# Optimization experiments

Measured on AMD Instinct MI355X. Metric: run time of the kernel, lower is better.

Reference implementation:

```python
import jax, jax.numpy as jnp
import numpy as np

B, NF, E, T, M = 4096, 50, 64, 2, 3
LN_EPS = 1e-5
NEG_INF = -1e9


def _xavier_uniform(k, shape, fan_in, fan_out):
    a = float(np.sqrt(6.0 / (fan_in + fan_out)))
    return jax.random.uniform(k, shape, jnp.float32, -a, a)


def setup_inputs() -> dict:
    key = jax.random.key(0)
    ks = jax.random.split(key, 6)
    feat = jax.random.normal(ks[0], (B, NF, E), jnp.float32)
    masker = _xavier_uniform(ks[1], (T, M, NF, NF), NF, NF)
    transform_w = _xavier_uniform(ks[2], (1, T, 1, 2 * E, E), 2 * E, E)
    transform_b = _xavier_uniform(ks[3], (T, 1, NF, E), NF, E)
    ln_w = jnp.ones((NF,), jnp.float32)
    ln_b = jnp.zeros((NF,), jnp.float32)
    gating_w = jax.random.normal(ks[4], (NF * E, 1), jnp.float32) / np.sqrt(NF * E)
    gating_b = jnp.zeros((1,), jnp.float32)
    return {
        "feat": feat,
        "masker": masker,
        "transform_w": transform_w,
        "transform_b": transform_b,
        "ln_w": ln_w,
        "ln_b": ln_b,
        "gating_w": gating_w,
        "gating_b": gating_b,
    }


def reference(feat, masker, transform_w, transform_b, ln_w, ln_b, gating_w, gating_b):
    b, nf, e = feat.shape
    t = masker.shape[0]
    # hop adjacency: product of masks, relu'd  (T, F, F)
    adj = jax.nn.relu(jnp.prod(masker, axis=1))
    mask = (adj != 0).astype(feat.dtype)
    # LayerNorm(num_fields) applied on transposed adj == normalize over axis -2,
    # with gamma/beta broadcasting along the normalized (row) axis.
    mean = adj.mean(axis=-2, keepdims=True)
    var = adj.var(axis=-2, keepdims=True)
    adj_ln = (adj - mean) / jnp.sqrt(var + LN_EPS) * ln_w[:, None] + ln_b[:, None]
    logits = adj_ln + (1.0 - mask) * NEG_INF + jnp.eye(nf, dtype=feat.dtype)
    # softmax over dim=1 of (T, F, F) == axis -2 (rows), then re-mask
    attn = jax.nn.softmax(logits, axis=-2) * mask
    # nei[b,t,g,e] = sum_f feat[b,f,e] * attn[t,f,g]
    nei = jnp.einsum('bfe,tfg->btge', feat, attn)  # (B, T, F, E)
    x = jnp.broadcast_to(feat[:, None], (b, t, nf, e))
    cat = jnp.concatenate([x, nei], axis=-1)  # (B, T, F, 2E)
    w0 = transform_w[0, :, 0]                 # (T, 2E, E)  (idx=0 slice)
    h = jnp.einsum('btfk,tke->btfe', cat, w0) + transform_b[:, 0]  # (B,T,F,E)
    flat = h.reshape(b, t, nf * e)
    gate = jax.nn.softmax(flat @ gating_w + gating_b, axis=1)  # (B, T, 1)
    out = jnp.sum(flat * gate, axis=1).reshape(b, nf, e)
    return out
```

## Files before the change

### kernel.cpp

```cpp
#include <hip/hip_runtime.h>
#include <hip/hip_bf16.h>

#define NFEAT 50
#define EDIM 64
#define LN_EPS 1e-5f
#define NEG_INF_C (-1000000000.0f)
#define NB 4

typedef __bf16 bf16_t;
typedef __bf16 bf16x8 __attribute__((ext_vector_type(8)));
typedef __bf16 bf16x4 __attribute__((ext_vector_type(4)));
typedef float f32x4 __attribute__((ext_vector_type(4)));


__global__ __launch_bounds__(256) void prep_kernel(
    const float* __restrict__ masker, const float* __restrict__ ln_w,
    const float* __restrict__ ln_b, const float* __restrict__ tw,
    const float* __restrict__ tb, const float* __restrict__ gw,
    bf16_t* __restrict__ ws_attnT, bf16_t* __restrict__ ws_WT,
    float* __restrict__ ws_tbT, float* __restrict__ ws_gwT,
    float* __restrict__ ws_cst)
{
  __shared__ float red[2][4];
  const int tid = threadIdx.x;
  const int lane = tid & 63;
  const int gidx = blockIdx.x * 256 + tid;

#pragma unroll
  for (int j = 0; j < 4; ++j) {
    int o = gidx * 4 + j;
    int kl = o & 63;
    int e = (o >> 6) & 63;
    int ti = o >> 12;
    int k = ((kl >> 3) ^ (e & 7)) * 8 + (kl & 7);
    ws_WT[o] = (bf16_t)tw[(ti * 64 + k) * 64 + e];
  }

#pragma unroll
  for (int j = 0; j < 2; ++j) {
    int o = gidx * 2 + j;
    int f = o & 63;
    int e = (o >> 6) & 63;
    int t = o >> 12;
    ws_tbT[o] = (f < NFEAT) ? tb[(t * NFEAT + f) * EDIM + e] : 0.f;
  }

  {
    int o = gidx;
    int f = o & 63;
    int e = o >> 6;
    ws_gwT[o] = (f < NFEAT) ? gw[f * EDIM + e] : 0.f;
  }

  if (blockIdx.x == 0) {
    float s0 = 0.f, s1 = 0.f;
    for (int i = tid; i < NFEAT * EDIM; i += 256) {
      float g = gw[i];
      s0 += tb[i] * g;
      s1 += tb[NFEAT * EDIM + i] * g;
    }
    for (int off = 32; off > 0; off >>= 1) {
      s0 += __shfl_xor(s0, off);
      s1 += __shfl_xor(s1, off);
    }
    if (lane == 0) { red[0][tid >> 6] = s0; red[1][tid >> 6] = s1; }
    __syncthreads();
    if (tid == 0) {
      ws_cst[0] = red[0][0] + red[0][1] + red[0][2] + red[0][3];
      ws_cst[1] = red[1][0] + red[1][1] + red[1][2] + red[1][3];
    }
  }

  const int wg = blockIdx.x * 4 + (tid >> 6);
  const int f = lane;
  const bool fv = (f < NFEAT);
  for (int i = 0; i < 2; ++i) {
    int col = wg * 2 + i;
    int t = col >> 6, g = col & 63;
    float val = 0.f;
    if (fv && g < NFEAT) {
      float a0 = masker[((t * 3 + 0) * NFEAT + f) * NFEAT + g];
      float a1 = masker[((t * 3 + 1) * NFEAT + f) * NFEAT + g];
      float a2 = masker[((t * 3 + 2) * NFEAT + f) * NFEAT + g];
      float prod = a0 * a1 * a2;
      val = prod > 0.f ? prod : 0.f;
    }
    float s = val;
    for (int off = 32; off > 0; off >>= 1) s += __shfl_xor(s, off);
    float mean = s / (float)NFEAT;
    float d = fv ? (val - mean) : 0.f;
    float v2 = d * d;
    for (int off = 32; off > 0; off >>= 1) v2 += __shfl_xor(v2, off);
    float var = v2 / (float)NFEAT;
    float lw = fv ? ln_w[f] : 0.f;
    float lb = fv ? ln_b[f] : 0.f;
    float aln = d * rsqrtf(var + LN_EPS) * lw + lb;
    float logit = aln + ((val != 0.f) ? 0.f : NEG_INF_C) + ((f == g) ? 1.f : 0.f);
    if (!fv) logit = -3.0e38f;
    float mx = logit;
    for (int off = 32; off > 0; off >>= 1) mx = fmaxf(mx, __shfl_xor(mx, off));
    float ex = fv ? expf(logit - mx) : 0.f;
    float se = ex;
    for (int off = 32; off > 0; off >>= 1) se += __shfl_xor(se, off);
    float attn = (fv && g < NFEAT && val != 0.f) ? (ex / se) : 0.f;
    ws_attnT[(t * 64 + g) * 64 + f] = (bf16_t)attn;
  }
}

__global__ __launch_bounds__(256) void main_kernel(
    const float* __restrict__ feat, const float* __restrict__ gb,
    const bf16_t* __restrict__ ws_attnT, const bf16_t* __restrict__ ws_WT,
    const float* __restrict__ ws_tbT, const float* __restrict__ ws_gwT,
    const float* __restrict__ ws_cst,
    float* __restrict__ out)
{
  __shared__ bf16_t sWT[4 * 64 * 64];
  __shared__ bf16_t sPT[2][64 * 72];
  __shared__ float sLog[2][4];

  const int tid = threadIdx.x;
  const int w = tid >> 6;
  const int lane = tid & 63;
  const int l16 = lane & 15;
  const int lquad = lane >> 4;
  const int m0 = w * 16;

#pragma unroll
  for (int it = 0; it < 8; ++it) {
    const int idx = it * 256 + tid;
    *(bf16x8*)&sWT[idx * 8] = *(const bf16x8*)(ws_WT + idx * 8);
  }

  bf16x8 aat[2][2];
#pragma unroll
  for (int t = 0; t < 2; ++t)
#pragma unroll
    for (int kc = 0; kc < 2; ++kc)
      aat[t][kc] = *(const bf16x8*)(ws_attnT + (t * 64 + m0 + l16) * 64 + kc * 32 + lquad * 8);

  const float cst0 = ws_cst[0], cst1 = ws_cst[1], gbv = gb[0];
  const int fA = m0 + l16;
  const bool fAv = (fA < NFEAT);
  const int b0 = blockIdx.x * NB;
  const int foff = fA * 64 + lquad * 8;
  const int exl = l16 & 7;

  f32x4 raw[4];
  if (fAv) {
    const float* fb = feat + b0 * (NFEAT * EDIM) + foff;
    raw[0] = *(const f32x4*)(fb);
    raw[1] = *(const f32x4*)(fb + 4);
    raw[2] = *(const f32x4*)(fb + 32);
    raw[3] = *(const f32x4*)(fb + 36);
  }

  __syncthreads();

#pragma unroll 1
  for (int ib = 0; ib < NB; ++ib) {
    const int b = b0 + ib;

    bf16x8 a[2];
#pragma unroll
    for (int kc = 0; kc < 2; ++kc)
#pragma unroll
      for (int j = 0; j < 8; ++j) a[kc][j] = (bf16_t)0.f;
    if (fAv) {
#pragma unroll
      for (int j = 0; j < 4; ++j) {
        a[0][j] = (bf16_t)raw[0][j]; a[0][j + 4] = (bf16_t)raw[1][j];
        a[1][j] = (bf16_t)raw[2][j]; a[1][j + 4] = (bf16_t)raw[3][j];
      }
    }

    if (ib + 1 < NB && fAv) {
      const float* fb = feat + (b + 1) * (NFEAT * EDIM) + foff;
      raw[0] = *(const f32x4*)(fb);
      raw[1] = *(const f32x4*)(fb + 4);
      raw[2] = *(const f32x4*)(fb + 32);
      raw[3] = *(const f32x4*)(fb + 36);
    }

    f32x4 accH[2][4], accP[2][4];
#pragma unroll
    for (int t = 0; t < 2; ++t)
#pragma unroll
      for (int n = 0; n < 4; ++n) {
        accH[t][n] = (f32x4){0.f, 0.f, 0.f, 0.f};
        accP[t][n] = (f32x4){0.f, 0.f, 0.f, 0.f};
      }

#pragma unroll
    for (int kc = 0; kc < 2; ++kc) {
      const int chunk = ((kc * 4 + lquad) ^ exl) * 8;
#pragma unroll
      for (int n = 0; n < 4; ++n) {
        const int ro = (n * 16 + l16) * 64 + chunk;
        const bf16x8 b10 = *(const bf16x8*)(&sWT[0 * 4096 + ro]);
        const bf16x8 b20 = *(const bf16x8*)(&sWT[1 * 4096 + ro]);
        const bf16x8 b11 = *(const bf16x8*)(&sWT[2 * 4096 + ro]);
        const bf16x8 b21 = *(const bf16x8*)(&sWT[3 * 4096 + ro]);
        accH[0][n] = __builtin_amdgcn_mfma_f32_16x16x32_bf16(a[kc], b10, accH[0][n], 0, 0, 0);
        accP[0][n] = __builtin_amdgcn_mfma_f32_16x16x32_bf16(a[kc], b20, accP[0][n], 0, 0, 0);
        accH[1][n] = __builtin_amdgcn_mfma_f32_16x16x32_bf16(a[kc], b11, accH[1][n], 0, 0, 0);
        accP[1][n] = __builtin_amdgcn_mfma_f32_16x16x32_bf16(a[kc], b21, accP[1][n], 0, 0, 0);
      }
    }

#pragma unroll
    for (int t = 0; t < 2; ++t)
#pragma unroll
      for (int n = 0; n < 4; ++n) {
        bf16x4 pv;
        pv[0] = (bf16_t)accP[t][n][0]; pv[1] = (bf16_t)accP[t][n][1];
        pv[2] = (bf16_t)accP[t][n][2]; pv[3] = (bf16_t)accP[t][n][3];
        *(bf16x4*)&sPT[t][(n * 16 + l16) * 72 + m0 + lquad * 4] = pv;
      }
    __syncthreads();

#pragma unroll
    for (int kc = 0; kc < 2; ++kc) {
#pragma unroll
      for (int n = 0; n < 4; ++n) {
        const int so = (n * 16 + l16) * 72 + kc * 32 + lquad * 8;
        const bf16x8 bp0 = *(const bf16x8*)(&sPT[0][so]);
        const bf16x8 bp1 = *(const bf16x8*)(&sPT[1][so]);
        accH[0][n] = __builtin_amdgcn_mfma_f32_16x16x32_bf16(aat[0][kc], bp0, accH[0][n], 0, 0, 0);
        accH[1][n] = __builtin_amdgcn_mfma_f32_16x16x32_bf16(aat[1][kc], bp1, accH[1][n], 0, 0, 0);
      }
    }

    float p0 = 0.f, p1 = 0.f;
#pragma unroll
    for (int n = 0; n < 4; ++n) {
      const f32x4 gwv = *(const f32x4*)(ws_gwT + (n * 16 + l16) * 64 + m0 + lquad * 4);
#pragma unroll
      for (int r = 0; r < 4; ++r) {
        p0 += accH[0][n][r] * gwv[r];
        p1 += accH[1][n][r] * gwv[r];
      }
    }
#pragma unroll
    for (int off = 32; off > 0; off >>= 1) {
      p0 += __shfl_xor(p0, off);
      p1 += __shfl_xor(p1, off);
    }
    if (lane == 0) { sLog[0][w] = p0; sLog[1][w] = p1; }
    __syncthreads();

    const float g0 = sLog[0][0] + sLog[0][1] + sLog[0][2] + sLog[0][3] + cst0 + gbv;
    const float g1 = sLog[1][0] + sLog[1][1] + sLog[1][2] + sLog[1][3] + cst1 + gbv;
    const float mx = fmaxf(g0, g1);
    const float e0 = expf(g0 - mx), e1 = expf(g1 - mx);
    const float inv = 1.f / (e0 + e1);
    const float ga0 = e0 * inv, ga1 = e1 * inv;

    float* outb = out + b * (NFEAT * EDIM);
#pragma unroll
    for (int n = 0; n < 4; ++n) {
      const int ro = (n * 16 + l16) * 64 + m0 + lquad * 4;
      const f32x4 tbv0 = *(const f32x4*)(ws_tbT + ro);
      const f32x4 tbv1 = *(const f32x4*)(ws_tbT + 64 * 64 + ro);
      const int e = n * 16 + l16;
#pragma unroll
      for (int r = 0; r < 4; ++r) {
        const int f = m0 + lquad * 4 + r;
        if (f < NFEAT)
          outb[f * 64 + e] = ga0 * (accH[0][n][r] + tbv0[r])
                           + ga1 * (accH[1][n][r] + tbv1[r]);
      }
    }
  }
}

extern "C" void kernel_launch(void* const* d_in, const int* in_sizes, int n_in,
                              void* d_out, int out_size, void* d_ws, size_t ws_size,
                              hipStream_t stream) {
  const float* feat   = (const float*)d_in[0];
  const float* masker = (const float*)d_in[1];
  const float* tw     = (const float*)d_in[2];
  const float* tb     = (const float*)d_in[3];
  const float* lnw    = (const float*)d_in[4];
  const float* lnb    = (const float*)d_in[5];
  const float* gw     = (const float*)d_in[6];
  const float* gb     = (const float*)d_in[7];
  float* out = (float*)d_out;

  bf16_t* ws_attnT = (bf16_t*)d_ws;
  bf16_t* ws_WT    = ws_attnT + 2 * 64 * 64;
  float*  ws_tbT   = (float*)(ws_WT + 4 * 64 * 64);
  float*  ws_gwT   = ws_tbT + 2 * 64 * 64;
  float*  ws_cst   = ws_gwT + 64 * 64;

  prep_kernel<<<16, 256, 0, stream>>>(masker, lnw, lnb, tw, tb, gw,
                                      ws_attnT, ws_WT, ws_tbT, ws_gwT, ws_cst);
  main_kernel<<<4096 / NB, 256, 0, stream>>>(feat, gb, ws_attnT, ws_WT,
                                             ws_tbT, ws_gwT, ws_cst, out);
}
```

Baseline: 138.1 us.

## Precompute gating projection matrix and split waves between H and P work

```diff
diff --git a/kernel.cpp b/kernel.cpp
--- a/kernel.cpp
+++ b/kernel.cpp
@@ -12,13 +12,15 @@
 typedef __bf16 bf16x4 __attribute__((ext_vector_type(4)));
 typedef float f32x4 __attribute__((ext_vector_type(4)));
 
+#define MFMA __builtin_amdgcn_mfma_f32_16x16x32_bf16
+
 
 __global__ __launch_bounds__(256) void prep_kernel(
     const float* __restrict__ masker, const float* __restrict__ ln_w,
     const float* __restrict__ ln_b, const float* __restrict__ tw,
     const float* __restrict__ tb, const float* __restrict__ gw,
     bf16_t* __restrict__ ws_attnT, bf16_t* __restrict__ ws_WT,
-    float* __restrict__ ws_tbT, float* __restrict__ ws_gwT,
+    float* __restrict__ ws_tbT, float* __restrict__ ws_attnF,
     float* __restrict__ ws_cst)
 {
   __shared__ float red[2][4];
@@ -43,13 +45,6 @@
     int e = (o >> 6) & 63;
     int t = o >> 12;
     ws_tbT[o] = (f < NFEAT) ? tb[(t * NFEAT + f) * EDIM + e] : 0.f;
-  }
-
-  {
-    int o = gidx;
-    int f = o & 63;
-    int e = o >> 6;
-    ws_gwT[o] = (f < NFEAT) ? gw[f * EDIM + e] : 0.f;
   }
 
   if (blockIdx.x == 0) {
@@ -104,26 +99,122 @@
     for (int off = 32; off > 0; off >>= 1) se += __shfl_xor(se, off);
     float attn = (fv && g < NFEAT && val != 0.f) ? (ex / se) : 0.f;
     ws_attnT[(t * 64 + g) * 64 + f] = (bf16_t)attn;
-  }
+    ws_attnF[(t * 64 + f) * 64 + g] = attn;
+  }
+}
+
+__global__ __launch_bounds__(256) void prep2_kernel(
+    const float* __restrict__ tw, const float* __restrict__ gw,
+    const float* __restrict__ ws_attnF, float* __restrict__ ws_G)
+{
+  __shared__ bf16_t sRT[64 * 72];
+  const int t = blockIdx.x;
+  const int tid = threadIdx.x;
+  const int w = tid >> 6;
+  const int lane = tid & 63;
+  const int l16 = lane & 15;
+  const int lquad = lane >> 4;
+  const int fr = w * 16 + l16;
+  const bool frv = (fr < NFEAT);
+
+  bf16x8 ag[2];
+#pragma unroll
+  for (int kc = 0; kc < 2; ++kc) {
+#pragma unroll
+    for (int j = 0; j < 8; ++j) ag[kc][j] = (bf16_t)0.f;
+    if (frv) {
+      const float* p = gw + fr * 64 + kc * 32 + lquad * 8;
+      const f32x4 r0 = *(const f32x4*)(p);
+      const f32x4 r1 = *(const f32x4*)(p + 4);
+#pragma unroll
+      for (int j = 0; j < 4; ++j) { ag[kc][j] = (bf16_t)r0[j]; ag[kc][j+4] = (bf16_t)r1[j]; }
+    }
+  }
+
+  f32x4 accR[4];
+#pragma unroll
+  for (int n = 0; n < 4; ++n) accR[n] = (f32x4){0.f,0.f,0.f,0.f};
+#pragma unroll
+  for (int kc = 0; kc < 2; ++kc)
+#pragma unroll
+    for (int n = 0; n < 4; ++n) {
+      const float* p = tw + ((2*t+1)*64 + n*16 + l16) * 64 + kc*32 + lquad*8;
+      const f32x4 r0 = *(const f32x4*)(p);
+      const f32x4 r1 = *(const f32x4*)(p + 4);
+      bf16x8 bw;
+#pragma unroll
+      for (int j = 0; j < 4; ++j) { bw[j] = (bf16_t)r0[j]; bw[j+4] = (bf16_t)r1[j]; }
+      accR[n] = MFMA(ag[kc], bw, accR[n], 0, 0, 0);
+    }
+#pragma unroll
+  for (int n = 0; n < 4; ++n) {
+    bf16x4 pv;
+    pv[0]=(bf16_t)accR[n][0]; pv[1]=(bf16_t)accR[n][1];
+    pv[2]=(bf16_t)accR[n][2]; pv[3]=(bf16_t)accR[n][3];
+    *(bf16x4*)&sRT[(n*16 + l16) * 72 + w*16 + lquad*4] = pv;
+  }
+
+  f32x4 acc[4];
+#pragma unroll
+  for (int n = 0; n < 4; ++n) acc[n] = (f32x4){0.f,0.f,0.f,0.f};
+#pragma unroll
+  for (int kc = 0; kc < 2; ++kc)
+#pragma unroll
+    for (int n = 0; n < 4; ++n) {
+      const float* p = tw + ((2*t)*64 + n*16 + l16) * 64 + kc*32 + lquad*8;
+      const f32x4 r0 = *(const f32x4*)(p);
+      const f32x4 r1 = *(const f32x4*)(p + 4);
+      bf16x8 bw;
+#pragma unroll
+      for (int j = 0; j < 4; ++j) { bw[j] = (bf16_t)r0[j]; bw[j+4] = (bf16_t)r1[j]; }
+      acc[n] = MFMA(ag[kc], bw, acc[n], 0, 0, 0);
+    }
+
+  __syncthreads();
+
+  bf16x8 aa[2];
+#pragma unroll
+  for (int kc = 0; kc < 2; ++kc) {
+    const float* p = ws_attnF + (t*64 + fr) * 64 + kc*32 + lquad*8;
+    const f32x4 r0 = *(const f32x4*)(p);
+    const f32x4 r1 = *(const f32x4*)(p + 4);
+#pragma unroll
+    for (int j = 0; j < 4; ++j) { aa[kc][j] = (bf16_t)r0[j]; aa[kc][j+4] = (bf16_t)r1[j]; }
+  }
+#pragma unroll
+  for (int kc = 0; kc < 2; ++kc)
+#pragma unroll
+    for (int n = 0; n < 4; ++n) {
+      const bf16x8 bp = *(const bf16x8*)(&sRT[(n*16 + l16) * 72 + kc*32 + lquad*8]);
+      acc[n] = MFMA(aa[kc], bp, acc[n], 0, 0, 0);
+    }
+
+#pragma unroll
+  for (int n = 0; n < 4; ++n)
+#pragma unroll
+    for (int r = 0; r < 4; ++r)
+      ws_G[t*4096 + (w*16 + lquad*4 + r) * 64 + n*16 + l16] = acc[n][r];
 }
 
 __global__ __launch_bounds__(256) void main_kernel(
     const float* __restrict__ feat, const float* __restrict__ gb,
     const bf16_t* __restrict__ ws_attnT, const bf16_t* __restrict__ ws_WT,
-    const float* __restrict__ ws_tbT, const float* __restrict__ ws_gwT,
+    const float* __restrict__ ws_tbT, const float* __restrict__ ws_G,
     const float* __restrict__ ws_cst,
     float* __restrict__ out)
 {
   __shared__ bf16_t sWT[4 * 64 * 64];
   __shared__ bf16_t sPT[2][64 * 72];
-  __shared__ float sLog[2][4];
+  __shared__ float sLog[2];
 
   const int tid = threadIdx.x;
   const int w = tid >> 6;
   const int lane = tid & 63;
   const int l16 = lane & 15;
   const int lquad = lane >> 4;
-  const int m0 = w * 16;
+  const bool isH = (w < 2);
+  const int pt = w - 2;
+  const int exl = l16 & 7;
 
 #pragma unroll
   for (int it = 0; it < 8; ++it) {
@@ -131,27 +222,40 @@
     *(bf16x8*)&sWT[idx * 8] = *(const bf16x8*)(ws_WT + idx * 8);
   }
 
-  bf16x8 aat[2][2];
-#pragma unroll
-  for (int t = 0; t < 2; ++t)
-#pragma unroll
-    for (int kc = 0; kc < 2; ++kc)
-      aat[t][kc] = *(const bf16x8*)(ws_attnT + (t * 64 + m0 + l16) * 64 + kc * 32 + lquad * 8);
+  bf16x8 aat[2][2][2];
+  if (isH) {
+#pragma unroll
+    for (int t = 0; t < 2; ++t)
+#pragma unroll
+      for (int kc = 0; kc < 2; ++kc)
+#pragma unroll
+        for (int ml = 0; ml < 2; ++ml)
+          aat[t][kc][ml] = *(const bf16x8*)(ws_attnT +
+              (t*64 + w*32 + ml*16 + l16) * 64 + kc*32 + lquad*8);
+  }
 
   const float cst0 = ws_cst[0], cst1 = ws_cst[1], gbv = gb[0];
-  const int fA = m0 + l16;
-  const bool fAv = (fA < NFEAT);
   const int b0 = blockIdx.x * NB;
-  const int foff = fA * 64 + lquad * 8;
-  const int exl = l16 & 7;
-
-  f32x4 raw[4];
-  if (fAv) {
-    const float* fb = feat + b0 * (NFEAT * EDIM) + foff;
-    raw[0] = *(const f32x4*)(fb);
-    raw[1] = *(const f32x4*)(fb + 4);
-    raw[2] = *(const f32x4*)(fb + 32);
-    raw[3] = *(const f32x4*)(fb + 36);
+  const int nm = isH ? 2 : 4;
+  const int fbase = isH ? w * 32 : 0;
+
+  f32x4 raw[16];
+#pragma unroll
+  for (int i = 0; i < 16; ++i) raw[i] = (f32x4){0.f,0.f,0.f,0.f};
+  {
+    const float* fb = feat + (long)b0 * (NFEAT * EDIM);
+#pragma unroll
+    for (int m = 0; m < 4; ++m)
+      if (m < nm) {
+        const int frow = fbase + m * 16 + l16;
+        if (frow < NFEAT) {
+          const float* p = fb + frow * 64 + lquad * 8;
+          raw[m*4+0] = *(const f32x4*)(p);
+          raw[m*4+1] = *(const f32x4*)(p + 4);
+          raw[m*4+2] = *(const f32x4*)(p + 32);
+          raw[m*4+3] = *(const f32x4*)(p + 36);
+        }
+      }
   }
 
   __syncthreads();
@@ -160,116 +264,141 @@
   for (int ib = 0; ib < NB; ++ib) {
     const int b = b0 + ib;
 
-    bf16x8 a[2];
+    bf16x8 a[2][4];
 #pragma unroll
     for (int kc = 0; kc < 2; ++kc)
 #pragma unroll
-      for (int j = 0; j < 8; ++j) a[kc][j] = (bf16_t)0.f;
-    if (fAv) {
-#pragma unroll
-      for (int j = 0; j < 4; ++j) {
-        a[0][j] = (bf16_t)raw[0][j]; a[0][j + 4] = (bf16_t)raw[1][j];
-        a[1][j] = (bf16_t)raw[2][j]; a[1][j + 4] = (bf16_t)raw[3][j];
+      for (int m = 0; m < 4; ++m)
+#pragma unroll
+        for (int j = 0; j < 4; ++j) {
+          a[kc][m][j]     = (bf16_t)raw[m*4 + kc*2][j];
+          a[kc][m][j + 4] = (bf16_t)raw[m*4 + kc*2 + 1][j];
+        }
+
+    if (!isH) {
+      const float* gt = ws_G + pt * 4096;
+      float p = 0.f;
+#pragma unroll
+      for (int m = 0; m < 4; ++m) {
+        const float* gp = gt + (m*16 + l16) * 64 + lquad * 8;
+        const f32x4 g0 = *(const f32x4*)(gp);
+        const f32x4 g1 = *(const f32x4*)(gp + 4);
+        const f32x4 g2 = *(const f32x4*)(gp + 32);
+        const f32x4 g3 = *(const f32x4*)(gp + 36);
+#pragma unroll
+        for (int j = 0; j < 4; ++j)
+          p += raw[m*4+0][j]*g0[j] + raw[m*4+1][j]*g1[j]
+             + raw[m*4+2][j]*g2[j] + raw[m*4+3][j]*g3[j];
       }
-    }
-
-    if (ib + 1 < NB && fAv) {
-      const float* fb = feat + (b + 1) * (NFEAT * EDIM) + foff;
-      raw[0] = *(const f32x4*)(fb);
-      raw[1] = *(const f32x4*)(fb + 4);
-      raw[2] = *(const f32x4*)(fb + 32);
-      raw[3] = *(const f32x4*)(fb + 36);
-    }
-
-    f32x4 accH[2][4], accP[2][4];
-#pragma unroll
-    for (int t = 0; t < 2; ++t)
-#pragma unroll
-      for (int n = 0; n < 4; ++n) {
-        accH[t][n] = (f32x4){0.f, 0.f, 0.f, 0.f};
-        accP[t][n] = (f32x4){0.f, 0.f, 0.f, 0.f};
+#pragma unroll
+      for (int off = 32; off > 0; off >>= 1) p += __shfl_xor(p, off);
+      if (lane == 0) sLog[pt] = p;
+    }
+
+    f32x4 acc[16];
+#pragma unroll
+    for (int i = 0; i < 16; ++i) acc[i] = (f32x4){0.f,0.f,0.f,0.f};
+
+    if (isH) {
+#pragma unroll
+      for (int kc = 0; kc < 2; ++kc) {
+        const int co = ((kc*4 + lquad) ^ exl) * 8;
+#pragma unroll
+        for (int n = 0; n < 4; ++n) {
+          const int ro = (n*16 + l16) * 64 + co;
+          const bf16x8 bw0 = *(const bf16x8*)(&sWT[0*4096 + ro]);
+          const bf16x8 bw1 = *(const bf16x8*)(&sWT[2*4096 + ro]);
+#pragma unroll
+          for (int ml = 0; ml < 2; ++ml) {
+            acc[ml*4 + n]     = MFMA(a[kc][ml], bw0, acc[ml*4 + n], 0, 0, 0);
+            acc[(2+ml)*4 + n] = MFMA(a[kc][ml], bw1, acc[(2+ml)*4 + n], 0, 0, 0);
+          }
+        }
       }
-
-#pragma unroll
-    for (int kc = 0; kc < 2; ++kc) {
-      const int chunk = ((kc * 4 + lquad) ^ exl) * 8;
-#pragma unroll
-      for (int n = 0; n < 4; ++n) {
-        const int ro = (n * 16 + l16) * 64 + chunk;
-        const bf16x8 b10 = *(const bf16x8*)(&sWT[0 * 4096 + ro]);
-        const bf16x8 b20 = *(const bf16x8*)(&sWT[1 * 4096 + ro]);
-        const bf16x8 b11 = *(const bf16x8*)(&sWT[2 * 4096 + ro]);
-        const bf16x8 b21 = *(const bf16x8*)(&sWT[3 * 4096 + ro]);
-        accH[0][n] = __builtin_amdgcn_mfma_f32_16x16x32_bf16(a[kc], b10, accH[0][n], 0, 0, 0);
-        accP[0][n] = __builtin_amdgcn_mfma_f32_16x16x32_bf16(a[kc], b20, accP[0][n], 0, 0, 0);
-        accH[1][n] = __builtin_amdgcn_mfma_f32_16x16x32_bf16(a[kc], b11, accH[1][n], 0, 0, 0);
-        accP[1][n] = __builtin_amdgcn_mfma_f32_16x16x32_bf16(a[kc], b21, accP[1][n], 0, 0, 0);
+    } else {
+      const int ti = 2*pt + 1;
+#pragma unroll
+      for (int kc = 0; kc < 2; ++kc) {
+        const int co = ((kc*4 + lquad) ^ exl) * 8;
+#pragma unroll
+        for (int n = 0; n < 4; ++n) {
+          const bf16x8 bw = *(const bf16x8*)(&sWT[ti*4096 + (n*16 + l16)*64 + co]);
+#pragma unroll
+          for (int m = 0; m < 4; ++m)
+            acc[m*4 + n] = MFMA(a[kc][m], bw, acc[m*4 + n], 0, 0, 0);
+        }
       }
-    }
-
-#pragma unroll
-    for (int t = 0; t < 2; ++t)
-#pragma unroll
-      for (int n = 0; n < 4; ++n) {
-        bf16x4 pv;
-        pv[0] = (bf16_t)accP[t][n][0]; pv[1] = (bf16_t)accP[t][n][1];
-        pv[2] = (bf16_t)accP[t][n][2]; pv[3] = (bf16_t)accP[t][n][3];
-        *(bf16x4*)&sPT[t][(n * 16 + l16) * 72 + m0 + lquad * 4] = pv;
-      }
+#pragma unroll
+      for (int m = 0; m < 4; ++m)
+#pragma unroll
+        for (int n = 0; n < 4; ++n) {
+          bf16x4 pv;
+          pv[0]=(bf16_t)acc[m*4+n][0]; pv[1]=(bf16_t)acc[m*4+n][1];
+          pv[2]=(bf16_t)acc[m*4+n][2]; pv[3]=(bf16_t)acc[m*4+n][3];
+          *(bf16x4*)&sPT[pt][(n*16 + l16) * 72 + m*16 + lquad*4] = pv;
+        }
+    }
+
     __syncthreads();
 
-#pragma unroll
-    for (int kc = 0; kc < 2; ++kc) {
-#pragma unroll
-      for (int n = 0; n < 4; ++n) {
-        const int so = (n * 16 + l16) * 72 + kc * 32 + lquad * 8;
-        const bf16x8 bp0 = *(const bf16x8*)(&sPT[0][so]);
-        const bf16x8 bp1 = *(const bf16x8*)(&sPT[1][so]);
-        accH[0][n] = __builtin_amdgcn_mfma_f32_16x16x32_bf16(aat[0][kc], bp0, accH[0][n], 0, 0, 0);
-        accH[1][n] = __builtin_amdgcn_mfma_f32_16x16x32_bf16(aat[1][kc], bp1, accH[1][n], 0, 0, 0);
-      }
-    }
-
-    float p0 = 0.f, p1 = 0.f;
-#pragma unroll
-    for (int n = 0; n < 4; ++n) {
-      const f32x4 gwv = *(const f32x4*)(ws_gwT + (n * 16 + l16) * 64 + m0 + lquad * 4);
-#pragma unroll
-      for (int r = 0; r < 4; ++r) {
-        p0 += accH[0][n][r] * gwv[r];
-        p1 += accH[1][n][r] * gwv[r];
-      }
-    }
-#pragma unroll
-    for (int off = 32; off > 0; off >>= 1) {
-      p0 += __shfl_xor(p0, off);
-      p1 += __shfl_xor(p1, off);
-    }
-    if (lane == 0) { sLog[0][w] = p0; sLog[1][w] = p1; }
+    if (ib + 1 < NB) {
+      const float* fb = feat + (long)(b + 1) * (NFEAT * EDIM);
+#pragma unroll
+      for (int m = 0; m < 4; ++m)
+        if (m < nm) {
+          const int frow = fbase + m * 16 + l16;
+          if (frow < NFEAT) {
+            const float* p = fb + frow * 64 + lquad * 8;
+            raw[m*4+0] = *(const f32x4*)(p);
+            raw[m*4+1] = *(const f32x4*)(p + 4);
+            raw[m*4+2] = *(const f32x4*)(p + 32);
+            raw[m*4+3] = *(const f32x4*)(p + 36);
+          }
+        }
+    }
+
+    if (isH) {
+      const float g0 = sLog[0] + cst0 + gbv;
+      const float g1 = sLog[1] + cst1 + gbv;
+      const float mx = fmaxf(g0, g1);
+      const float e0 = expf(g0 - mx), e1 = expf(g1 - mx);
+      const float inv = 1.f / (e0 + e1);
+      const float ga0 = e0 * inv, ga1 = e1 * inv;
+
+#pragma unroll
+      for (int kc = 0; kc < 2; ++kc)
+#pragma unroll
+        for (int n = 0; n < 4; ++n) {
+          const int so = (n*16 + l16) * 72 + kc*32 + lquad*8;
+          const bf16x8 bp0 = *(const bf16x8*)(&sPT[0][so]);
+          const bf16x8 bp1 = *(const bf16x8*)(&sPT[1][so]);
+#pragma unroll
+          for (int ml = 0; ml < 2; ++ml) {
+            acc[ml*4 + n]     = MFMA(aat[0][kc][ml], bp0, acc[ml*4 + n], 0, 0, 0);
+            acc[(2+ml)*4 + n] = MFMA(aat[1][kc][ml], bp1, acc[(2+ml)*4 + n], 0, 0, 0);
+          }
+        }
+
+      float* outb = out + (long)b * (NFEAT * EDIM);
+#pragma unroll
+      for (int ml = 0; ml < 2; ++ml)
+#pragma unroll
+        for (int n = 0; n < 4; ++n) {
+          const int fo = w*32 + ml*16 + lquad*4;
+          const f32x4 tb0 = *(const f32x4*)(ws_tbT + (n*16 + l16)*64 + fo);
+          const f32x4 tb1 = *(const f32x4*)(ws_tbT + 4096 + (n*16 + l16)*64 + fo);
+          const int e = n*16 + l16;
+#pragma unroll
+          for (int r = 0; r < 4; ++r) {
+            const int f = fo + r;
+            if (f < NFEAT)
+              outb[f*64 + e] = ga0 * (acc[ml*4 + n][r] + tb0[r])
+                             + ga1 * (acc[(2+ml)*4 + n][r] + tb1[r]);
+          }
+        }
+    }
+
     __syncthreads();
-
-    const float g0 = sLog[0][0] + sLog[0][1] + sLog[0][2] + sLog[0][3] + cst0 + gbv;
-    const float g1 = sLog[1][0] + sLog[1][1] + sLog[1][2] + sLog[1][3] + cst1 + gbv;
-    const float mx = fmaxf(g0, g1);
-    const float e0 = expf(g0 - mx), e1 = expf(g1 - mx);
-    const float inv = 1.f / (e0 + e1);
-    const float ga0 = e0 * inv, ga1 = e1 * inv;
-
-    float* outb = out + b * (NFEAT * EDIM);
-#pragma unroll
-    for (int n = 0; n < 4; ++n) {
-      const int ro = (n * 16 + l16) * 64 + m0 + lquad * 4;
-      const f32x4 tbv0 = *(const f32x4*)(ws_tbT + ro);
-      const f32x4 tbv1 = *(const f32x4*)(ws_tbT + 64 * 64 + ro);
-      const int e = n * 16 + l16;
-#pragma unroll
-      for (int r = 0; r < 4; ++r) {
-        const int f = m0 + lquad * 4 + r;
-        if (f < NFEAT)
-          outb[f * 64 + e] = ga0 * (accH[0][n][r] + tbv0[r])
-                           + ga1 * (accH[1][n][r] + tbv1[r]);
-      }
-    }
   }
 }
 
@@ -287,13 +416,15 @@
   float* out = (float*)d_out;
 
   bf16_t* ws_attnT = (bf16_t*)d_ws;
-  bf16_t* ws_WT    = ws_attnT + 2 * 64 * 64;
-  float*  ws_tbT   = (float*)(ws_WT + 4 * 64 * 64);
-  float*  ws_gwT   = ws_tbT + 2 * 64 * 64;
-  float*  ws_cst   = ws_gwT + 64 * 64;
+  bf16_t* ws_WT    = ws_attnT + 8192;
+  float*  ws_tbT   = (float*)(ws_WT + 16384);
+  float*  ws_attnF = ws_tbT + 8192;
+  float*  ws_G     = ws_attnF + 8192;
+  float*  ws_cst   = ws_G + 8192;
 
   prep_kernel<<<16, 256, 0, stream>>>(masker, lnw, lnb, tw, tb, gw,
-                                      ws_attnT, ws_WT, ws_tbT, ws_gwT, ws_cst);
+                                      ws_attnT, ws_WT, ws_tbT, ws_attnF, ws_cst);
+  prep2_kernel<<<2, 256, 0, stream>>>(tw, gw, ws_attnF, ws_G);
   main_kernel<<<4096 / NB, 256, 0, stream>>>(feat, gb, ws_attnT, ws_WT,
-                                             ws_tbT, ws_gwT, ws_cst, out);
+                                             ws_tbT, ws_G, ws_cst, out);
 }
```

New measurement: 241.8 us. +75.1%, slower.
